# Performance work log

Measured on AMD Instinct MI355X. Metric: run time of the kernel, lower is better.

The kernel has to match this reference:

```python
import jax, jax.numpy as jnp
import numpy as np

NEG_SLOPE = 0.2  # PyG GATConv default negative_slope
N_NODES = 100000


def gat_conv(x, W, a_src, a_dst, src, dst, n_nodes):
    """One PyG-style GATConv (eval mode, self-loops already in src/dst).
    x: [N, in], W: [in, H*O], a_src/a_dst: [H, O]. Returns [N, H, O]."""
    heads, out_ch = a_src.shape
    h = (x @ W).reshape(n_nodes, heads, out_ch)          # [N,H,O]
    al_src = jnp.einsum('nho,ho->nh', h, a_src)          # [N,H]
    al_dst = jnp.einsum('nho,ho->nh', h, a_dst)          # [N,H]
    e = jax.nn.leaky_relu(al_src[src] + al_dst[dst], NEG_SLOPE)  # [E,H]
    # segment softmax over incoming edges of each dst node
    m = jax.ops.segment_max(e, dst, num_segments=n_nodes)       # [N,H]
    e = jnp.exp(e - m[dst])
    denom = jax.ops.segment_sum(e, dst, num_segments=n_nodes)   # [N,H]
    alpha = e / denom[dst]                                       # [E,H]
    msg = h[src] * alpha[:, :, None]                             # [E,H,O]
    return jax.ops.segment_sum(msg, dst, num_segments=n_nodes)  # [N,H,O]


def setup_inputs() -> dict:
    key = jax.random.key(0)
    ks = jax.random.split(key, 10)
    N, E = N_NODES, 3200000
    node_attr_dim, state_dim, heads, out_dim = 128, 8, 8, 1
    hid = state_dim * heads  # 64

    def glorot(k, shape, fan_in, fan_out):
        return jax.random.normal(k, shape, dtype=jnp.float32) * np.sqrt(2.0 / (fan_in + fan_out)).astype(np.float32)

    x = jax.random.normal(ks[0], (N, node_attr_dim), dtype=jnp.float32)
    edge_index = jax.random.randint(ks[1], (2, E), 0, N, dtype=jnp.int64)
    W1 = glorot(ks[2], (node_attr_dim, heads * state_dim), node_attr_dim, heads * state_dim)
    a_src1 = glorot(ks[3], (heads, state_dim), state_dim, 1)
    a_dst1 = glorot(ks[4], (heads, state_dim), state_dim, 1)
    b1 = jnp.zeros((hid,), dtype=jnp.float32)
    W2 = glorot(ks[5], (hid, out_dim), hid, out_dim)
    a_src2 = glorot(ks[6], (1, out_dim), out_dim, 1)
    a_dst2 = glorot(ks[7], (1, out_dim), out_dim, 1)
    b2 = jnp.zeros((out_dim,), dtype=jnp.float32)
    return {"x": x, "W1": W1, "a_src1": a_src1, "a_dst1": a_dst1, "b1": b1,
            "W2": W2, "a_src2": a_src2, "a_dst2": a_dst2, "b2": b2,
            "edge_index": edge_index}


def reference(x, W1, a_src1, a_dst1, b1, W2, a_src2, a_dst2, b2, edge_index):
    n = N_NODES
    loops = jnp.arange(n, dtype=edge_index.dtype)
    src = jnp.concatenate([edge_index[0], loops])  # add self-loops (PyG default)
    dst = jnp.concatenate([edge_index[1], loops])
    # layer 1: heads=8, concat -> [N, 64]
    h1 = gat_conv(x, W1, a_src1, a_dst1, src, dst, n)
    h1 = h1.reshape(n, -1) + b1
    h1 = jax.nn.relu(h1)  # dropout skipped (eval)
    # layer 2: heads=1, concat(size 1) -> [N, 1]
    h2 = gat_conv(h1, W2, a_src2, a_dst2, src, dst, n)
    out = h2.reshape(n, -1) + b2
    return out
```

## Files before the change

### kernel.cpp

```cpp
#include <hip/hip_runtime.h>
#include <math.h>

#define NEG 0.2f
#define CHUNK 16384

__device__ __forceinline__ float lrelu(float v) { return fmaxf(v, NEG * v); }

__device__ __forceinline__ unsigned short f2bf(float f) {
    unsigned u = __float_as_uint(f);
    u = (u + 0x7fffu + ((u >> 16) & 1u)) >> 16;
    return (unsigned short)u;
}
__device__ __forceinline__ float bf2f(unsigned short s) {
    return __uint_as_float((unsigned)s << 16);
}

__global__ __launch_bounds__(256) void k1(const float* __restrict__ x,
        const float* __restrict__ W1, const float* __restrict__ a_src,
        const float* __restrict__ a_dst,
        unsigned short* __restrict__ h1b, float* __restrict__ als,
        float* __restrict__ ald, int N)
{
    __shared__ float Wl[128 * 64];
    __shared__ float xt[128][68];

    const int tid = threadIdx.x;
    const int base = blockIdx.x * 64;

    const float4* Wv = (const float4*)W1;
    float4* Wlv = (float4*)Wl;
    for (int i = tid; i < 128 * 16; i += 256) Wlv[i] = Wv[i];

    for (int idx = tid; idx < 64 * 32; idx += 256) {
        int nl = idx >> 5;
        int k4 = (idx & 31) * 4;
        int n = base + nl;
        float4 v = make_float4(0.f, 0.f, 0.f, 0.f);
        if (n < N) v = *(const float4*)&x[(size_t)n * 128 + k4];
        xt[k4 + 0][nl] = v.x;
        xt[k4 + 1][nl] = v.y;
        xt[k4 + 2][nl] = v.z;
        xt[k4 + 3][nl] = v.w;
    }
    __syncthreads();

    const int wave = tid >> 6, lane = tid & 63;
    const int g = lane >> 4, c = lane & 15;
    const int nl0 = wave * 16 + 4 * g;

    float acc[4][4];
    #pragma unroll
    for (int j = 0; j < 4; ++j)
        #pragma unroll
        for (int t = 0; t < 4; ++t) acc[j][t] = 0.f;

    #pragma unroll 4
    for (int k = 0; k < 128; ++k) {
        float4 wv = *(const float4*)&Wl[k * 64 + 4 * c];
        float4 xv = *(const float4*)&xt[k][nl0];
        const float xs[4] = {xv.x, xv.y, xv.z, xv.w};
        const float wsv[4] = {wv.x, wv.y, wv.z, wv.w};
        #pragma unroll
        for (int j = 0; j < 4; ++j)
            #pragma unroll
            for (int t = 0; t < 4; ++t)
                acc[j][t] = fmaf(xs[j], wsv[t], acc[j][t]);
    }

    float a_s[4], a_d[4];
    #pragma unroll
    for (int t = 0; t < 4; ++t) { a_s[t] = a_src[4 * c + t]; a_d[t] = a_dst[4 * c + t]; }

    #pragma unroll
    for (int j = 0; j < 4; ++j) {
        int n = base + nl0 + j;
        float ps = 0.f, pd = 0.f;
        #pragma unroll
        for (int t = 0; t < 4; ++t) {
            ps = fmaf(acc[j][t], a_s[t], ps);
            pd = fmaf(acc[j][t], a_d[t], pd);
        }
        ps += __shfl_xor(ps, 1, 64);
        pd += __shfl_xor(pd, 1, 64);
        if (n < N) {
            ushort4 hb;
            hb.x = f2bf(acc[j][0]); hb.y = f2bf(acc[j][1]);
            hb.z = f2bf(acc[j][2]); hb.w = f2bf(acc[j][3]);
            *(ushort4*)&h1b[(size_t)n * 64 + 4 * c] = hb;
            if ((c & 1) == 0) {
                als[n * 8 + (c >> 1)] = ps;
                ald[n * 8 + (c >> 1)] = pd;
            }
        }
    }
}


__global__ __launch_bounds__(256) void p1(const int* __restrict__ ei, int E, int N,
        int* __restrict__ T, int NB, int NC)
{
    extern __shared__ int hist[];
    int tid = threadIdx.x;
    for (int b = tid; b < NB; b += 256) hist[b] = 0;
    __syncthreads();
    int base = blockIdx.x * CHUNK;
    for (int i = tid; i < CHUNK; i += 256) {
        int e = base + i;
        if (e >= E) break;
        int d = ei[E + e];
        if ((unsigned)d < (unsigned)N) atomicAdd(&hist[d >> 8], 1);
    }
    __syncthreads();
    for (int b = tid; b < NB; b += 256) T[b * NC + blockIdx.x] = hist[b];
}

__global__ __launch_bounds__(256) void p2a(int* __restrict__ T,
        int* __restrict__ total, int NB, int NC)
{
    int wave = threadIdx.x >> 6, lane = threadIdx.x & 63;
    int b = blockIdx.x * 4 + wave;
    if (b >= NB) return;
    int run = 0;
    for (int j0 = 0; j0 < NC; j0 += 64) {
        int j = j0 + lane;
        int orig = (j < NC) ? T[b * NC + j] : 0;
        int v = orig;
        #pragma unroll
        for (int off = 1; off < 64; off <<= 1) {
            int t = __shfl_up(v, off, 64);
            if (lane >= off) v += t;
        }
        if (j < NC) T[b * NC + j] = run + v - orig;
        run += __shfl(v, 63, 64);
    }
    if (lane == 0) total[b] = run;
}

__global__ __launch_bounds__(512) void p2b(const int* __restrict__ total,
        int* __restrict__ bstart, int nb)
{
    __shared__ int s[512];
    int tid = threadIdx.x;
    int run = 0;
    for (int base = 0; base < nb; base += 512) {
        int i = base + tid;
        int orig = (i < nb) ? total[i] : 0;
        s[tid] = orig;
        __syncthreads();
        #pragma unroll
        for (int off = 1; off < 512; off <<= 1) {
            int t = (tid >= off) ? s[tid - off] : 0;
            __syncthreads();
            s[tid] += t;
            __syncthreads();
        }
        if (i < nb) bstart[i] = run + s[tid] - orig;
        int tot = s[511];
        __syncthreads();
        run += tot;
    }
    if (tid == 0) bstart[nb] = run;
}

__global__ __launch_bounds__(256) void p3(const int* __restrict__ ei, int E, int N,
        const int* __restrict__ T, const int* __restrict__ bstart,
        unsigned* __restrict__ tmp, int NB, int NC)
{
    extern __shared__ int cur[];
    int tid = threadIdx.x;
    int j = blockIdx.x;
    for (int b = tid; b < NB; b += 256) cur[b] = bstart[b] + T[b * NC + j];
    __syncthreads();
    int base = j * CHUNK;
    for (int i = tid; i < CHUNK; i += 256) {
        int e = base + i;
        if (e >= E) break;
        int d = ei[E + e];
        if ((unsigned)d >= (unsigned)N) continue;
        int s = ei[e];
        if ((unsigned)s >= (unsigned)N) s = 0;
        int pos = atomicAdd(&cur[d >> 8], 1);
        if ((unsigned)pos < (unsigned)E)
            tmp[pos] = (unsigned)s | ((unsigned)(d & 255) << 24);
    }
}

__global__ __launch_bounds__(256) void p4(const unsigned* __restrict__ tmp,
        const int* __restrict__ bstart,
        int* __restrict__ cnt, int* __restrict__ rowptr, int* __restrict__ csr,
        int N, int E)
{
    __shared__ int hist[256];
    __shared__ int ssc[256];
    __shared__ int cur[256];
    int tid = threadIdx.x;
    int b = blockIdx.x;
    int s0 = bstart[b], s1 = bstart[b + 1];
    if (s0 < 0) s0 = 0; if (s0 > E) s0 = E;
    if (s1 < s0) s1 = s0; if (s1 > E) s1 = E;

    hist[tid] = 0;
    __syncthreads();
    for (int i = s0 + tid; i < s1; i += 256)
        atomicAdd(&hist[tmp[i] >> 24], 1);
    __syncthreads();

    int h = hist[tid];
    ssc[tid] = h;
    __syncthreads();
    #pragma unroll
    for (int off = 1; off < 256; off <<= 1) {
        int t = (tid >= off) ? ssc[tid - off] : 0;
        __syncthreads();
        ssc[tid] += t;
        __syncthreads();
    }
    int excl = ssc[tid] - h;
    int node = b * 256 + tid;
    if (node < N) {
        cnt[node] = h;
        rowptr[node] = s0 + excl;
    }
    cur[tid] = s0 + excl;
    __syncthreads();

    for (int i = s0 + tid; i < s1; i += 256) {
        unsigned v = tmp[i];
        int pos = atomicAdd(&cur[v >> 24], 1);
        if ((unsigned)pos < (unsigned)E) csr[pos] = (int)(v & 0xFFFFFFu);
    }
}


__global__ __launch_bounds__(256) void kh(const int* __restrict__ ei, int E, int N,
                                          int* __restrict__ cnt)
{
    int e = blockIdx.x * 256 + threadIdx.x;
    if (e >= E) return;
    int d = ei[E + e];
    if ((unsigned)d < (unsigned)N) atomicAdd(&cnt[d], 1);
}

__global__ __launch_bounds__(256) void ka(const int* __restrict__ cnt,
        int* __restrict__ rowptr, int* __restrict__ cursor,
        int* __restrict__ gtotal, int N)
{
    __shared__ int s[256];
    __shared__ int base;
    int tid = threadIdx.x;
    int g = blockIdx.x * 256 + tid;
    int v = (g < N) ? cnt[g] : 0;
    s[tid] = v;
    __syncthreads();
    #pragma unroll
    for (int off = 1; off < 256; off <<= 1) {
        int t = (tid >= off) ? s[tid - off] : 0;
        __syncthreads();
        s[tid] += t;
        __syncthreads();
    }
    if (tid == 255) base = atomicAdd(gtotal, s[255]);
    __syncthreads();
    if (g < N) {
        int r = base + s[tid] - v;
        rowptr[g] = r;
        cursor[g] = r;
    }
}

__global__ __launch_bounds__(256) void kc(const int* __restrict__ ei, int E, int N,
        int* __restrict__ cursor, int* __restrict__ csr)
{
    int e = blockIdx.x * 256 + threadIdx.x;
    if (e >= E) return;
    int s = ei[e];
    int d = ei[E + e];
    if ((unsigned)d >= (unsigned)N) return;
    int p = atomicAdd(&cursor[d], 1);
    if ((unsigned)p < (unsigned)E) csr[p] = s;
}


__global__ __launch_bounds__(256) void g1(const int* __restrict__ csr,
        const int* __restrict__ rowptr, const int* __restrict__ cnt,
        const unsigned short* __restrict__ h1b, const float* __restrict__ als,
        const float* __restrict__ ald,
        const float* __restrict__ b1, const float* __restrict__ W2,
        const float* __restrict__ a_src2, const float* __restrict__ a_dst2,
        float2* __restrict__ h2a, float* __restrict__ ald2, int N, int E)
{
    int wave = threadIdx.x >> 6, lane = threadIdx.x & 63;
    int n = blockIdx.x * 4 + wave;
    if (n >= N) return;
    int h = lane >> 3;

    float ald_h = ald[n * 8 + h];
    float hv = bf2f(h1b[(size_t)n * 64 + lane]);
    float w = __expf(lrelu(als[n * 8 + h] + ald_h));
    float den = w;
    float acc = w * hv;

    int start = rowptr[n];
    int c = cnt[n];
    if ((unsigned)start >= (unsigned)E) { start = 0; c = 0; }
    if (c < 0) c = 0;
    if (start + c > E) c = E - start;

    for (int cbase = 0; cbase < c; cbase += 64) {
        int rem = c - cbase; if (rem > 64) rem = 64;
        int sv = 0;
        if (lane < rem) {
            int t = csr[start + cbase + lane];
            if ((unsigned)t < (unsigned)N) sv = t;
        }
        int i = 0;
        for (; i + 4 <= rem; i += 4) {
            int s0 = __shfl(sv, i + 0, 64);
            int s1 = __shfl(sv, i + 1, 64);
            int s2 = __shfl(sv, i + 2, 64);
            int s3 = __shfl(sv, i + 3, 64);
            float a0 = als[s0 * 8 + h];
            float a1 = als[s1 * 8 + h];
            float a2 = als[s2 * 8 + h];
            float a3 = als[s3 * 8 + h];
            unsigned short u0 = h1b[s0 * 64 + lane];
            unsigned short u1 = h1b[s1 * 64 + lane];
            unsigned short u2 = h1b[s2 * 64 + lane];
            unsigned short u3 = h1b[s3 * 64 + lane];
            float w0 = __expf(lrelu(a0 + ald_h));
            float w1 = __expf(lrelu(a1 + ald_h));
            float w2 = __expf(lrelu(a2 + ald_h));
            float w3 = __expf(lrelu(a3 + ald_h));
            den += (w0 + w1) + (w2 + w3);
            acc = fmaf(w0, bf2f(u0), acc);
            acc = fmaf(w1, bf2f(u1), acc);
            acc = fmaf(w2, bf2f(u2), acc);
            acc = fmaf(w3, bf2f(u3), acc);
        }
        for (; i < rem; ++i) {
            int s0 = __shfl(sv, i, 64);
            float a0 = als[s0 * 8 + h];
            unsigned short u0 = h1b[s0 * 64 + lane];
            float w0 = __expf(lrelu(a0 + ald_h));
            den += w0;
            acc = fmaf(w0, bf2f(u0), acc);
        }
    }

    float v = fmaxf(acc / den + b1[lane], 0.f);
    float t = v * W2[lane];
    #pragma unroll
    for (int off = 1; off < 64; off <<= 1) t += __shfl_xor(t, off, 64);
    if (lane == 0) {
        float2 p;
        p.x = t;
        p.y = t * a_src2[0];
        h2a[n] = p;
        ald2[n] = t * a_dst2[0];
    }
}

__global__ __launch_bounds__(256) void g2(const int* __restrict__ csr,
        const int* __restrict__ rowptr, const int* __restrict__ cnt,
        const float2* __restrict__ h2a, const float* __restrict__ ald2,
        const float* __restrict__ b2, float* __restrict__ out, int N, int E)
{
    int sub = threadIdx.x >> 5;
    int l32 = threadIdx.x & 31;
    int n = blockIdx.x * 8 + sub;
    if (n >= N) return;

    float ad = ald2[n];
    int start = rowptr[n];
    int c = cnt[n];
    if ((unsigned)start >= (unsigned)E) { start = 0; c = 0; }
    if (c < 0) c = 0;
    if (start + c > E) c = E - start;

    float den = 0.f, acc = 0.f;
    for (int i = l32; i < c; i += 32) {
        int src = csr[start + i];
        if ((unsigned)src >= (unsigned)N) src = 0;
        float2 p = h2a[src];
        float w = __expf(lrelu(p.y + ad));
        den += w;
        acc = fmaf(w, p.x, acc);
    }
    #pragma unroll
    for (int off = 1; off < 32; off <<= 1) {
        den += __shfl_xor(den, off, 32);
        acc += __shfl_xor(acc, off, 32);
    }
    if (l32 == 0) {
        float2 p = h2a[n];
        float w0 = __expf(lrelu(p.y + ad));
        out[n] = (acc + w0 * p.x) / (den + w0) + b2[0];
    }
}

extern "C" void kernel_launch(void* const* d_in, const int* in_sizes, int n_in,
                              void* d_out, int out_size, void* d_ws, size_t ws_size,
                              hipStream_t stream)
{
    const float* x   = (const float*)d_in[0];
    const float* W1  = (const float*)d_in[1];
    const float* as1 = (const float*)d_in[2];
    const float* ad1 = (const float*)d_in[3];
    const float* b1  = (const float*)d_in[4];
    const float* W2  = (const float*)d_in[5];
    const float* as2 = (const float*)d_in[6];
    const float* ad2 = (const float*)d_in[7];
    const float* b2  = (const float*)d_in[8];
    const int*   ei  = (const int*)d_in[9];

    int N = in_sizes[0] / 128;
    int E = in_sizes[9] / 2;
    int NB = (N + 255) >> 8;
    int NC = (E + CHUNK - 1) / CHUNK;

    char* wsb = (char*)d_ws;
    size_t off = 0;
    auto alloc = [&](size_t bytes) -> char* {
        char* p = wsb + off;
        off = (off + bytes + 255) & ~(size_t)255;
        return p;
    };

    unsigned short* h1b = (unsigned short*)alloc((size_t)N * 64 * 2);
    float* als    = (float*)alloc((size_t)N * 8 * 4);
    float* ald    = (float*)alloc((size_t)N * 8 * 4);
    float2* h2a   = (float2*)alloc((size_t)N * 8);
    float* ald2   = (float*)alloc((size_t)N * 4);
    int* cnt      = (int*)alloc((size_t)N * 4);
    int* rowptr   = (int*)alloc((size_t)N * 4);
    int* csr      = (int*)alloc((size_t)E * 4);
    size_t common = off;

    int* T        = (int*)alloc((size_t)NB * NC * 4);
    int* total    = (int*)alloc((size_t)NB * 4);
    int* bstart   = (int*)alloc((size_t)(NB + 1) * 4);
    unsigned* tmp = (unsigned*)alloc((size_t)E * 4);
    size_t need_new = off;

    k1<<<(N + 63) / 64, 256, 0, stream>>>(x, W1, as1, ad1, h1b, als, ald, N);

    if (ws_size >= need_new && NB <= 512) {
        size_t lds = (size_t)NB * 4;
        p1<<<NC, 256, lds, stream>>>(ei, E, N, T, NB, NC);
        p2a<<<(NB + 3) / 4, 256, 0, stream>>>(T, total, NB, NC);
        p2b<<<1, 512, 0, stream>>>(total, bstart, NB);
        p3<<<NC, 256, lds, stream>>>(ei, E, N, T, bstart, tmp, NB, NC);
        p4<<<NB, 256, 0, stream>>>(tmp, bstart, cnt, rowptr, csr, N, E);
    } else {
        off = common;
        int* gtotal = (int*)alloc(32);
        int* cursor = (int*)alloc((size_t)N * 4);
        hipMemsetAsync(cnt, 0, (size_t)N * sizeof(int), stream);
        hipMemsetAsync(gtotal, 0, 32, stream);
        kh<<<(E + 255) / 256, 256, 0, stream>>>(ei, E, N, cnt);
        ka<<<(N + 255) / 256, 256, 0, stream>>>(cnt, rowptr, cursor, gtotal, N);
        kc<<<(E + 255) / 256, 256, 0, stream>>>(ei, E, N, cursor, csr);
    }

    g1<<<(N + 3) / 4, 256, 0, stream>>>(csr, rowptr, cnt, h1b, als, ald,
                                        b1, W2, as2, ad2, h2a, ald2, N, E);
    g2<<<(N + 7) / 8, 256, 0, stream>>>(csr, rowptr, cnt, h2a, ald2, b2,
                                        (float*)d_out, N, E);
}
```

Baseline: 393.3 us.

## Restructure layer-1 gather: compute each edge weight once, split wave into two edge halves

The layer-1 aggregation kernel now computes each edge's attention exponent once per (edge, head), with 8 edges by 8 heads spread over the wave, instead of redundantly in all 8 lanes of a head. The h1 row is read as packed 32-bit bf16 pairs by 32 lanes, and the two half-waves process alternate edges and are summed at the end. Weights and source offsets are broadcast with shuffles. This cuts exp and als loads by 8x and halves gather instruction count, at the cost of extra shuffles and a more complex reduction.

```diff
diff --git a/kernel.cpp b/kernel.cpp
--- a/kernel.cpp
+++ b/kernel.cpp
@@ -280,7 +280,6 @@
     if ((unsigned)p < (unsigned)E) csr[p] = s;
 }
 
-
 __global__ __launch_bounds__(256) void g1(const int* __restrict__ csr,
         const int* __restrict__ rowptr, const int* __restrict__ cnt,
         const unsigned short* __restrict__ h1b, const float* __restrict__ als,
@@ -289,22 +288,32 @@
         const float* __restrict__ a_src2, const float* __restrict__ a_dst2,
         float2* __restrict__ h2a, float* __restrict__ ald2, int N, int E)
 {
-    int wave = threadIdx.x >> 6, lane = threadIdx.x & 63;
-    int n = blockIdx.x * 4 + wave;
+    const int wave = threadIdx.x >> 6, lane = threadIdx.x & 63;
+    const int n = blockIdx.x * 4 + wave;
     if (n >= N) return;
-    int h = lane >> 3;
-
-    float ald_h = ald[n * 8 + h];
-    float hv = bf2f(h1b[(size_t)n * 64 + lane]);
-    float w = __expf(lrelu(als[n * 8 + h] + ald_h));
-    float den = w;
-    float acc = w * hv;
+
+    const int s = lane >> 5;
+    const int cp = lane & 31;
+    const int hp = cp >> 2;
+    const int eslot = lane >> 3;
+    const int hw = lane & 7;
+
+    const unsigned* h1w = (const unsigned*)h1b;
+
+    const float ald_hw = ald[n * 8 + hw];
+    float denp = 0.f;
+    float acc0 = 0.f, acc1 = 0.f;
 
     int start = rowptr[n];
     int c = cnt[n];
     if ((unsigned)start >= (unsigned)E) { start = 0; c = 0; }
     if (c < 0) c = 0;
     if (start + c > E) c = E - start;
+
+    int wi0 = (2 * 0 + s) * 8 + hp;
+    int wi1 = (2 * 1 + s) * 8 + hp;
+    int wi2 = (2 * 2 + s) * 8 + hp;
+    int wi3 = (2 * 3 + s) * 8 + hp;
 
     for (int cbase = 0; cbase < c; cbase += 64) {
         int rem = c - cbase; if (rem > 64) rem = 64;
@@ -313,44 +322,51 @@
             int t = csr[start + cbase + lane];
             if ((unsigned)t < (unsigned)N) sv = t;
         }
-        int i = 0;
-        for (; i + 4 <= rem; i += 4) {
-            int s0 = __shfl(sv, i + 0, 64);
-            int s1 = __shfl(sv, i + 1, 64);
-            int s2 = __shfl(sv, i + 2, 64);
-            int s3 = __shfl(sv, i + 3, 64);
-            float a0 = als[s0 * 8 + h];
-            float a1 = als[s1 * 8 + h];
-            float a2 = als[s2 * 8 + h];
-            float a3 = als[s3 * 8 + h];
-            unsigned short u0 = h1b[s0 * 64 + lane];
-            unsigned short u1 = h1b[s1 * 64 + lane];
-            unsigned short u2 = h1b[s2 * 64 + lane];
-            unsigned short u3 = h1b[s3 * 64 + lane];
-            float w0 = __expf(lrelu(a0 + ald_h));
-            float w1 = __expf(lrelu(a1 + ald_h));
-            float w2 = __expf(lrelu(a2 + ald_h));
-            float w3 = __expf(lrelu(a3 + ald_h));
-            den += (w0 + w1) + (w2 + w3);
-            acc = fmaf(w0, bf2f(u0), acc);
-            acc = fmaf(w1, bf2f(u1), acc);
-            acc = fmaf(w2, bf2f(u2), acc);
-            acc = fmaf(w3, bf2f(u3), acc);
-        }
-        for (; i < rem; ++i) {
-            int s0 = __shfl(sv, i, 64);
-            float a0 = als[s0 * 8 + h];
-            unsigned short u0 = h1b[s0 * 64 + lane];
-            float w0 = __expf(lrelu(a0 + ald_h));
-            den += w0;
-            acc = fmaf(w0, bf2f(u0), acc);
-        }
-    }
-
-    float v = fmaxf(acc / den + b1[lane], 0.f);
-    float t = v * W2[lane];
-    #pragma unroll
-    for (int off = 1; off < 64; off <<= 1) t += __shfl_xor(t, off, 64);
+        for (int g0 = 0; g0 < rem; g0 += 8) {
+            int ge = g0 + eslot;
+            int esrc = __shfl(sv, ge, 64);
+            float wv = 0.f;
+            if (ge < rem)
+                wv = __expf(lrelu(als[esrc * 8 + hw] + ald_hw));
+            denp += wv;
+            int eoff = esrc << 5;
+
+            int nr = rem - g0; if (nr > 8) nr = 8;
+            #pragma unroll
+            for (int r = 0; r < 4; ++r) {
+                if (2 * r >= nr) break;
+                int wi = (r == 0) ? wi0 : (r == 1) ? wi1 : (r == 2) ? wi2 : wi3;
+                float fw = __shfl(wv, wi, 64);
+                int fo = __shfl(eoff, wi, 64);
+                unsigned u = h1w[fo + cp];
+                acc0 = fmaf(fw, __uint_as_float(u << 16), acc0);
+                acc1 = fmaf(fw, __uint_as_float(u & 0xffff0000u), acc1);
+            }
+        }
+    }
+
+    float dsum = denp;
+    dsum += __shfl_xor(dsum, 8, 64);
+    dsum += __shfl_xor(dsum, 16, 64);
+    dsum += __shfl_xor(dsum, 32, 64);
+    float den = __shfl(dsum, hp, 64);
+
+    acc0 += __shfl_xor(acc0, 32, 64);
+    acc1 += __shfl_xor(acc1, 32, 64);
+
+    float wsf = __expf(lrelu(als[n * 8 + hp] + ald[n * 8 + hp]));
+    unsigned un = h1w[(n << 5) + cp];
+    den += wsf;
+    acc0 = fmaf(wsf, __uint_as_float(un << 16), acc0);
+    acc1 = fmaf(wsf, __uint_as_float(un & 0xffff0000u), acc1);
+
+    float2 bb = *(const float2*)&b1[2 * cp];
+    float2 w2 = *(const float2*)&W2[2 * cp];
+    float v0 = fmaxf(acc0 / den + bb.x, 0.f);
+    float v1 = fmaxf(acc1 / den + bb.y, 0.f);
+    float t = fmaf(v0, w2.x, v1 * w2.y);
+    #pragma unroll
+    for (int off = 1; off < 32; off <<= 1) t += __shfl_xor(t, off, 64);
     if (lane == 0) {
         float2 p;
         p.x = t;
```

Measured after the change: 433.4 us. +10.2%, slower.
